# Kernel tuning notes

Measured on AMD Instinct MI355X. Metric: run time of the kernel, lower is better.

The kernel has to match this reference:

```python
import jax, jax.numpy as jnp
import numpy as np

EPS = 1e-5

def _bn(h, gamma, beta):
    # BatchNorm1d in training mode: per-channel stats over the batch dim (L=1)
    m = jnp.mean(h, axis=0)
    v = jnp.var(h, axis=0)  # biased variance, as torch uses for normalization
    return gamma * (h - m) * jax.lax.rsqrt(v + EPS) + beta

def setup_inputs() -> dict:
    key = jax.random.key(0)
    ks = jax.random.split(key, 8)
    vocab, emb = 8192, 512
    inter = (vocab + emb) // 2  # 4352
    N = 8192
    x_t = jax.random.randint(ks[0], (N,), 0, vocab, dtype=jnp.int64)
    W1 = jax.random.normal(ks[1], (inter, vocab), dtype=jnp.float32) * 0.02
    b1 = jax.random.normal(ks[2], (inter,), dtype=jnp.float32) * 0.02
    g1 = jnp.ones((inter,), dtype=jnp.float32)
    beta1 = jnp.zeros((inter,), dtype=jnp.float32)
    W2 = jax.random.normal(ks[3], (emb, inter), dtype=jnp.float32) * 0.02
    b2 = jax.random.normal(ks[4], (emb,), dtype=jnp.float32) * 0.02
    g2 = jnp.ones((emb,), dtype=jnp.float32)
    beta2 = jnp.zeros((emb,), dtype=jnp.float32)
    return {"x_t": x_t, "W1": W1, "b1": b1, "g1": g1, "beta1": beta1,
            "W2": W2, "b2": b2, "g2": g2, "beta2": beta2}

def reference(x_t, W1, b1, g1, beta1, W2, b2, g2, beta2):
    # one_hot(x_t) @ Conv1d(k=1) weight == gather of W1 columns (same math, no dense one-hot)
    h1 = W1.T[x_t] + b1                      # [N, inter]
    h1 = jax.nn.gelu(_bn(h1, g1, beta1), approximate=False)
    h2 = h1 @ W2.T + b2                      # [N, emb]
    out = jax.nn.gelu(_bn(h2, g2, beta2), approximate=False)
    return out
```

## Files before the change

### kernel.cpp

```cpp
#include <hip/hip_runtime.h>
#include <hip/hip_bf16.h>
#include <math.h>

typedef __attribute__((ext_vector_type(8))) short short8;
typedef __attribute__((ext_vector_type(4))) float f32x4;

#define VOCAB 8192
#define NSAMP 8192
#define INTER 4352
#define EMB   512

#define OFF_CNT    0
#define OFF_A1     32768
#define OFF_M1     50176
#define OFF_A2     67584
#define OFF_M2     69632
#define OFF_PS1B   71680
#define OFF_DONE   333824
#define OFF_PS2B   1120256
#define OFF_W2B    2168832
#define OFF_HACT   6625280
#define OFF_H2     77928448

__device__ __forceinline__ float gelu_exact(float x) {
    return 0.5f * x * (1.0f + erff(x * 0.70710678118654752f));
}
__device__ __forceinline__ unsigned short f2bf(float x) {
    __hip_bfloat16 b = __float2bfloat16(x);
    return *reinterpret_cast<unsigned short*>(&b);
}
__device__ __forceinline__ void async16(const unsigned short* g, unsigned short* l) {
    __builtin_amdgcn_global_load_lds(
        (const __attribute__((address_space(1))) void*)g,
        (__attribute__((address_space(3))) void*)l, 16, 0, 0);
}

__global__ __launch_bounds__(1024) void k_hist1b(const int* __restrict__ xt,
                                                 int* __restrict__ cnt,
                                                 unsigned* __restrict__ done) {
    __shared__ int h[VOCAB];
    const int t = threadIdx.x;
    #pragma unroll
    for (int i = 0; i < 8; ++i) h[t + i * 1024] = 0;
    if (t == 0) *done = 0u;
    __syncthreads();
    const int4* x4 = (const int4*)xt;
    int4 a = x4[t], b = x4[t + 1024];
    atomicAdd(&h[a.x], 1); atomicAdd(&h[a.y], 1);
    atomicAdd(&h[a.z], 1); atomicAdd(&h[a.w], 1);
    atomicAdd(&h[b.x], 1); atomicAdd(&h[b.y], 1);
    atomicAdd(&h[b.z], 1); atomicAdd(&h[b.w], 1);
    __syncthreads();
    #pragma unroll
    for (int i = 0; i < 2; ++i)
        ((int4*)cnt)[t + i * 1024] = ((const int4*)h)[t + i * 1024];
}

__global__ __launch_bounds__(256) void k_stats1(const float* __restrict__ W1,
                                                const int* __restrict__ cnt,
                                                const float* __restrict__ g1,
                                                float* __restrict__ a1,
                                                float* __restrict__ m1) {
    const int t = threadIdx.x, lane = t & 63, w = t >> 6;
    const int row = blockIdx.x * 4 + w;
    const float* wr = W1 + (size_t)row * VOCAB;
    float s1 = 0.f, s2 = 0.f;
    #pragma unroll 8
    for (int it = 0; it < 32; ++it) {
        int v = it * 256 + lane * 4;
        float4 x = *(const float4*)(wr + v);
        int4 c = *(const int4*)(cnt + v);
        float cx = (float)c.x, cy = (float)c.y, cz = (float)c.z, cw = (float)c.w;
        s1 += cx * x.x + cy * x.y + cz * x.z + cw * x.w;
        s2 += cx * x.x * x.x + cy * x.y * x.y + cz * x.z * x.z + cw * x.w * x.w;
    }
    #pragma unroll
    for (int d = 1; d < 64; d <<= 1) {
        s1 += __shfl_xor(s1, d);
        s2 += __shfl_xor(s2, d);
    }
    if (lane == 0) {
        float m = s1 * (1.f / NSAMP);
        float var = s2 * (1.f / NSAMP) - m * m;
        a1[row] = g1[row] * rsqrtf(var + 1e-5f);
        m1[row] = m;
    }
}

__global__ __launch_bounds__(256) void k_buildw2(const float* __restrict__ W1,
                                                 const float* __restrict__ a1,
                                                 const float* __restrict__ m1,
                                                 const float* __restrict__ beta1,
                                                 unsigned short* __restrict__ Hact,
                                                 const float* __restrict__ W2,
                                                 unsigned short* __restrict__ W2b) {
    const int bx = blockIdx.x;
    const int t = threadIdx.x;
    if (bx >= 2176) {
        int idx = ((bx - 2176) * 256 + t) * 4;
        float4 w = *(const float4*)(W2 + idx);
        ushort4 u;
        u.x = f2bf(w.x); u.y = f2bf(w.y); u.z = f2bf(w.z); u.w = f2bf(w.w);
        *(ushort4*)(W2b + idx) = u;
        return;
    }
    const int i0 = (bx % 68) * 64;
    const int v0 = (bx / 68) * 256;
    const int c0 = (t & 15) * 4;
    const int vg = (t >> 4) * 4;
    float4 av = *(const float4*)(a1 + i0 + c0);
    float4 mv = *(const float4*)(m1 + i0 + c0);
    float4 bv = *(const float4*)(beta1 + i0 + c0);
    const float* ap = (const float*)&av;
    const float* mp = (const float*)&mv;
    const float* bp = (const float*)&bv;
    #pragma unroll
    for (int vi = 0; vi < 4; ++vi) {
        int vb = v0 + vi * 64 + vg;
        float wf[4][4];
        #pragma unroll
        for (int j = 0; j < 4; ++j)
            *(float4*)&wf[j][0] = *(const float4*)(W1 + (size_t)(i0 + c0 + j) * VOCAB + vb);
        #pragma unroll
        for (int k = 0; k < 4; ++k) {
            ushort4 o;
            o.x = f2bf(gelu_exact(ap[0] * (wf[0][k] - mp[0]) + bp[0]));
            o.y = f2bf(gelu_exact(ap[1] * (wf[1][k] - mp[1]) + bp[1]));
            o.z = f2bf(gelu_exact(ap[2] * (wf[2][k] - mp[2]) + bp[2]));
            o.w = f2bf(gelu_exact(ap[3] * (wf[3][k] - mp[3]) + bp[3]));
            *(ushort4*)&Hact[(size_t)(vb + k) * INTER + i0 + c0] = o;
        }
    }
}

__global__ __launch_bounds__(256) void k_gemm(const unsigned short* __restrict__ A,
                                              const unsigned short* __restrict__ B,
                                              const int* __restrict__ cnt,
                                              float* __restrict__ h2,
                                              float* __restrict__ ps1,
                                              float* __restrict__ ps2,
                                              const float* __restrict__ g2,
                                              float* __restrict__ a2,
                                              float* __restrict__ m2,
                                              unsigned* __restrict__ done) {
    __shared__ __align__(16) unsigned short sA[2][128 * 64];
    __shared__ __align__(16) unsigned short sB[2][64 * 64];
    const int bid = blockIdx.x;
    const int mblk = bid & 63;
    const int nblk = bid >> 6;
    const int m0 = mblk * 128;
    const int n0 = nblk * 64;
    const int t = threadIdx.x;
    const int lane = t & 63;
    const int wave = t >> 6;
    const int wr = wave >> 1, wc = wave & 1;
    const int mq = lane & 15, kq = lane >> 4;
    const int srow = lane >> 3;
    const int sgrp = lane & 7;
    const int scol = (sgrp ^ srow) * 8;
    const int swz = mq & 7;

    const unsigned short* Ab = A + (size_t)(m0 + wave * 32 + srow) * INTER + scol;
    const unsigned short* Bb = B + (size_t)(n0 + wave * 16 + srow) * INTER + scol;

    f32x4 acc[4][2];
    #pragma unroll
    for (int r = 0; r < 4; ++r)
        #pragma unroll
        for (int c = 0; c < 2; ++c) acc[r][c] = (f32x4){0.f, 0.f, 0.f, 0.f};

    auto stage = [&](int buf, int tile) {
        const int k0 = tile * 64;
        #pragma unroll
        for (int p = 0; p < 4; ++p)
            async16(Ab + (size_t)(p * 8) * INTER + k0, &sA[buf][(wave * 32 + p * 8) * 64]);
        #pragma unroll
        for (int p = 0; p < 2; ++p)
            async16(Bb + (size_t)(p * 8) * INTER + k0, &sB[buf][(wave * 16 + p * 8) * 64]);
    };
    auto compute = [&](int buf) {
        #pragma unroll
        for (int kk = 0; kk < 64; kk += 32) {
            const int gbase = kq + (kk >> 3);
            short8 af[4], bfr[2];
            #pragma unroll
            for (int r = 0; r < 4; ++r)
                af[r] = *(const short8*)&sA[buf][(wr * 64 + r * 16 + mq) * 64 + ((gbase ^ swz) * 8)];
            #pragma unroll
            for (int c = 0; c < 2; ++c)
                bfr[c] = *(const short8*)&sB[buf][(wc * 32 + c * 16 + mq) * 64 + ((gbase ^ swz) * 8)];
            __builtin_amdgcn_s_setprio(1);
            #pragma unroll
            for (int r = 0; r < 4; ++r)
                #pragma unroll
                for (int c = 0; c < 2; ++c)
                    acc[r][c] = __builtin_amdgcn_mfma_f32_16x16x32_bf16(af[r], bfr[c], acc[r][c], 0, 0, 0);
            __builtin_amdgcn_s_setprio(0);
        }
    };

    stage(0, 0);
    __syncthreads();
    #pragma unroll 1
    for (int ti = 0; ti < 67; ++ti) {
        stage((ti + 1) & 1, ti + 1);
        compute(ti & 1);
        __syncthreads();
    }
    compute(1);

    float s1[2] = {0.f, 0.f}, s2[2] = {0.f, 0.f};
    #pragma unroll
    for (int r = 0; r < 4; ++r) {
        const int rowb = m0 + wr * 64 + r * 16 + kq * 4;
        int4 cw = *(const int4*)(cnt + rowb);
        float w0 = (float)cw.x, w1 = (float)cw.y, w2 = (float)cw.z, w3 = (float)cw.w;
        #pragma unroll
        for (int c = 0; c < 2; ++c) {
            const int col = n0 + wc * 32 + c * 16 + mq;
            float v0 = acc[r][c][0], v1 = acc[r][c][1], v2 = acc[r][c][2], v3 = acc[r][c][3];
            h2[(size_t)(rowb + 0) * EMB + col] = v0;
            h2[(size_t)(rowb + 1) * EMB + col] = v1;
            h2[(size_t)(rowb + 2) * EMB + col] = v2;
            h2[(size_t)(rowb + 3) * EMB + col] = v3;
            s1[c] += w0 * v0 + w1 * v1 + w2 * v2 + w3 * v3;
            s2[c] += w0 * v0 * v0 + w1 * v1 * v1 + w2 * v2 * v2 + w3 * v3 * v3;
        }
    }
    #pragma unroll
    for (int c = 0; c < 2; ++c) {
        s1[c] += __shfl_xor(s1[c], 16);
        s2[c] += __shfl_xor(s2[c], 16);
        s1[c] += __shfl_xor(s1[c], 32);
        s2[c] += __shfl_xor(s2[c], 32);
    }
    if (lane < 16) {
        const int slot = mblk * 2 + wr;
        #pragma unroll
        for (int c = 0; c < 2; ++c) {
            const int col = n0 + wc * 32 + c * 16 + mq;
            ps1[(size_t)col * 128 + slot] = s1[c];
            ps2[(size_t)col * 128 + slot] = s2[c];
        }
    }

    __shared__ bool sLast;
    __syncthreads();
    if (t == 0) {
        __threadfence();
        sLast = (atomicAdd(done, 1u) == 511u);
    }
    __syncthreads();
    if (sLast) {
        __threadfence();
        #pragma unroll
        for (int e = t; e < 512; e += 256) {
            float f1 = 0.f, f2 = 0.f;
            const float4* p1 = (const float4*)(ps1 + (size_t)e * 128);
            const float4* p2 = (const float4*)(ps2 + (size_t)e * 128);
            #pragma unroll 8
            for (int i = 0; i < 32; ++i) {
                float4 u = p1[i]; f1 += u.x + u.y + u.z + u.w;
                float4 v = p2[i]; f2 += v.x + v.y + v.z + v.w;
            }
            float m = f1 * (1.f / NSAMP);
            float var = f2 * (1.f / NSAMP) - m * m;
            a2[e] = g2[e] * rsqrtf(var + 1e-5f);
            m2[e] = m;
        }
    }
}

__global__ __launch_bounds__(256) void k_final(const float* __restrict__ h2,
                                               const int* __restrict__ xt,
                                               const float* __restrict__ a2,
                                               const float* __restrict__ m2,
                                               const float* __restrict__ beta2,
                                               float* __restrict__ out) {
    const int t = threadIdx.x;
    const int n = blockIdx.x * 2 + (t >> 7);
    const int e = (t & 127) * 4;
    const int v = xt[n];
    float4 h = *(const float4*)(h2 + (size_t)v * EMB + e);
    float4 a = *(const float4*)(a2 + e);
    float4 m = *(const float4*)(m2 + e);
    float4 b = *(const float4*)(beta2 + e);
    float4 o;
    o.x = gelu_exact(a.x * (h.x - m.x) + b.x);
    o.y = gelu_exact(a.y * (h.y - m.y) + b.y);
    o.z = gelu_exact(a.z * (h.z - m.z) + b.z);
    o.w = gelu_exact(a.w * (h.w - m.w) + b.w);
    *(float4*)(out + (size_t)n * EMB + e) = o;
}

extern "C" void kernel_launch(void* const* d_in, const int* in_sizes, int n_in,
                              void* d_out, int out_size, void* d_ws, size_t ws_size,
                              hipStream_t stream) {
    const int* xt      = (const int*)d_in[0];
    const float* W1    = (const float*)d_in[1];
    const float* g1    = (const float*)d_in[3];
    const float* beta1 = (const float*)d_in[4];
    const float* W2    = (const float*)d_in[5];
    const float* g2    = (const float*)d_in[7];
    const float* beta2 = (const float*)d_in[8];
    float* out = (float*)d_out;

    char* ws = (char*)d_ws;
    int*   cnt  = (int*)  (ws + OFF_CNT);
    float* a1   = (float*)(ws + OFF_A1);
    float* m1   = (float*)(ws + OFF_M1);
    float* a2   = (float*)(ws + OFF_A2);
    float* m2   = (float*)(ws + OFF_M2);
    float* ps1b = (float*)(ws + OFF_PS1B);
    float* ps2b = (float*)(ws + OFF_PS2B);
    unsigned* done = (unsigned*)(ws + OFF_DONE);
    unsigned short* W2b  = (unsigned short*)(ws + OFF_W2B);
    unsigned short* Hact = (unsigned short*)(ws + OFF_HACT);
    float* h2   = (float*)(ws + OFF_H2);

    k_hist1b<<<1, 1024, 0, stream>>>(xt, cnt, done);
    k_stats1<<<1088, 256, 0, stream>>>(W1, cnt, g1, a1, m1);
    k_buildw2<<<4352, 256, 0, stream>>>(W1, a1, m1, beta1, Hact, W2, W2b);
    k_gemm<<<512, 256, 0, stream>>>(Hact, W2b, cnt, h2, ps1b, ps2b, g2, a2, m2, done);
    k_final<<<4096, 256, 0, stream>>>(h2, xt, a2, m2, beta2, out);
}
```

Baseline: 368.4 us.

## Split GEMM over K with two partials and last-arriver reduction; larger N tile

The bf16 GEMM now uses a 128x128 tile with 512 threads and can split the K dimension in two. Each split writes its own partial output, and the second block to arrive for a tile sums both partials and runs the epilogue (stats and the h2 write). The single-block histogram kernel is replaced by a global-atomic histogram plus memsets, and h2 rows with zero count are no longer written. The aim is more blocks in flight and less per-block serial K work, at the cost of writing and reading an extra partial buffer, more atomics and two extra launches.

```diff
diff --git a/kernel.cpp b/kernel.cpp
--- a/kernel.cpp
+++ b/kernel.cpp
@@ -16,11 +16,12 @@
 #define OFF_A2     67584
 #define OFF_M2     69632
 #define OFF_PS1B   71680
-#define OFF_DONE   333824
+#define OFF_FLAGS  333824
 #define OFF_PS2B   1120256
 #define OFF_W2B    2168832
 #define OFF_HACT   6625280
 #define OFF_H2     77928448
+#define PART_BYTES 16777216ULL
 
 __device__ __forceinline__ float gelu_exact(float x) {
     return 0.5f * x * (1.0f + erff(x * 0.70710678118654752f));
@@ -35,25 +36,9 @@
         (__attribute__((address_space(3))) void*)l, 16, 0, 0);
 }
 
-__global__ __launch_bounds__(1024) void k_hist1b(const int* __restrict__ xt,
-                                                 int* __restrict__ cnt,
-                                                 unsigned* __restrict__ done) {
-    __shared__ int h[VOCAB];
-    const int t = threadIdx.x;
-    #pragma unroll
-    for (int i = 0; i < 8; ++i) h[t + i * 1024] = 0;
-    if (t == 0) *done = 0u;
-    __syncthreads();
-    const int4* x4 = (const int4*)xt;
-    int4 a = x4[t], b = x4[t + 1024];
-    atomicAdd(&h[a.x], 1); atomicAdd(&h[a.y], 1);
-    atomicAdd(&h[a.z], 1); atomicAdd(&h[a.w], 1);
-    atomicAdd(&h[b.x], 1); atomicAdd(&h[b.y], 1);
-    atomicAdd(&h[b.z], 1); atomicAdd(&h[b.w], 1);
-    __syncthreads();
-    #pragma unroll
-    for (int i = 0; i < 2; ++i)
-        ((int4*)cnt)[t + i * 1024] = ((const int4*)h)[t + i * 1024];
+__global__ void k_hist(const int* __restrict__ xt, int* __restrict__ cnt) {
+    int n = blockIdx.x * 256 + threadIdx.x;
+    atomicAdd(&cnt[xt[n]], 1);
 }
 
 __global__ __launch_bounds__(256) void k_stats1(const float* __restrict__ W1,
@@ -133,35 +118,41 @@
     }
 }
 
-__global__ __launch_bounds__(256) void k_gemm(const unsigned short* __restrict__ A,
+__global__ __launch_bounds__(512) void k_gemm(const unsigned short* __restrict__ A,
                                               const unsigned short* __restrict__ B,
                                               const int* __restrict__ cnt,
+                                              float* __restrict__ hpart,
                                               float* __restrict__ h2,
                                               float* __restrict__ ps1,
                                               float* __restrict__ ps2,
                                               const float* __restrict__ g2,
                                               float* __restrict__ a2,
                                               float* __restrict__ m2,
-                                              unsigned* __restrict__ done) {
+                                              unsigned* __restrict__ flags,
+                                              int kPer, int S) {
     __shared__ __align__(16) unsigned short sA[2][128 * 64];
-    __shared__ __align__(16) unsigned short sB[2][64 * 64];
+    __shared__ __align__(16) unsigned short sB[2][128 * 64];
     const int bid = blockIdx.x;
     const int mblk = bid & 63;
-    const int nblk = bid >> 6;
+    const int nblk = (bid >> 6) & 3;
+    const int ks   = bid >> 8;
     const int m0 = mblk * 128;
-    const int n0 = nblk * 64;
+    const int n0 = nblk * 128;
+    const int kbeg = ks * kPer;
+    const int nsteps = kPer >> 6;
+    float* C = hpart + (size_t)ks * NSAMP * EMB;
     const int t = threadIdx.x;
     const int lane = t & 63;
     const int wave = t >> 6;
-    const int wr = wave >> 1, wc = wave & 1;
+    const int wr = wave >> 2, wc = wave & 3;
     const int mq = lane & 15, kq = lane >> 4;
     const int srow = lane >> 3;
     const int sgrp = lane & 7;
     const int scol = (sgrp ^ srow) * 8;
     const int swz = mq & 7;
 
-    const unsigned short* Ab = A + (size_t)(m0 + wave * 32 + srow) * INTER + scol;
-    const unsigned short* Bb = B + (size_t)(n0 + wave * 16 + srow) * INTER + scol;
+    const unsigned short* Ab = A + (size_t)(m0 + wave * 16 + srow) * INTER + kbeg + scol;
+    const unsigned short* Bb = B + (size_t)(n0 + wave * 16 + srow) * INTER + kbeg + scol;
 
     f32x4 acc[4][2];
     #pragma unroll
@@ -171,12 +162,10 @@
 
     auto stage = [&](int buf, int tile) {
         const int k0 = tile * 64;
-        #pragma unroll
-        for (int p = 0; p < 4; ++p)
-            async16(Ab + (size_t)(p * 8) * INTER + k0, &sA[buf][(wave * 32 + p * 8) * 64]);
-        #pragma unroll
-        for (int p = 0; p < 2; ++p)
-            async16(Bb + (size_t)(p * 8) * INTER + k0, &sB[buf][(wave * 16 + p * 8) * 64]);
+        async16(Ab + k0,                     &sA[buf][(wave * 16) * 64]);
+        async16(Ab + (size_t)8 * INTER + k0, &sA[buf][(wave * 16 + 8) * 64]);
+        async16(Bb + k0,                     &sB[buf][(wave * 16) * 64]);
+        async16(Bb + (size_t)8 * INTER + k0, &sB[buf][(wave * 16 + 8) * 64]);
     };
     auto compute = [&](int buf) {
         #pragma unroll
@@ -202,29 +191,60 @@
     stage(0, 0);
     __syncthreads();
     #pragma unroll 1
-    for (int ti = 0; ti < 67; ++ti) {
+    for (int ti = 0; ti < nsteps - 1; ++ti) {
         stage((ti + 1) & 1, ti + 1);
         compute(ti & 1);
         __syncthreads();
     }
-    compute(1);
-
+    compute((nsteps - 1) & 1);
+
+    #pragma unroll
+    for (int r = 0; r < 4; ++r) {
+        const int rowb = m0 + wr * 64 + r * 16 + kq * 4;
+        #pragma unroll
+        for (int c = 0; c < 2; ++c) {
+            const int col = n0 + wc * 32 + c * 16 + mq;
+            #pragma unroll
+            for (int j = 0; j < 4; ++j)
+                C[(size_t)(rowb + j) * EMB + col] = acc[r][c][j];
+        }
+    }
+
+    __shared__ bool sLoser, sLast;
+    if (S == 2) {
+        __syncthreads();
+        if (t == 0) {
+            __threadfence();
+            sLoser = (atomicAdd(&flags[bid & 255], 1u) == 1u);
+        }
+        __syncthreads();
+        if (!sLoser) return;
+        __threadfence();
+    }
+
+    const float* other = hpart + (size_t)(1 - ks) * NSAMP * EMB;
     float s1[2] = {0.f, 0.f}, s2[2] = {0.f, 0.f};
     #pragma unroll
     for (int r = 0; r < 4; ++r) {
         const int rowb = m0 + wr * 64 + r * 16 + kq * 4;
         int4 cw = *(const int4*)(cnt + rowb);
-        float w0 = (float)cw.x, w1 = (float)cw.y, w2 = (float)cw.z, w3 = (float)cw.w;
         #pragma unroll
         for (int c = 0; c < 2; ++c) {
             const int col = n0 + wc * 32 + c * 16 + mq;
             float v0 = acc[r][c][0], v1 = acc[r][c][1], v2 = acc[r][c][2], v3 = acc[r][c][3];
-            h2[(size_t)(rowb + 0) * EMB + col] = v0;
-            h2[(size_t)(rowb + 1) * EMB + col] = v1;
-            h2[(size_t)(rowb + 2) * EMB + col] = v2;
-            h2[(size_t)(rowb + 3) * EMB + col] = v3;
-            s1[c] += w0 * v0 + w1 * v1 + w2 * v2 + w3 * v3;
-            s2[c] += w0 * v0 * v0 + w1 * v1 * v1 + w2 * v2 * v2 + w3 * v3 * v3;
+            if (S == 2) {
+                v0 += other[(size_t)(rowb + 0) * EMB + col];
+                v1 += other[(size_t)(rowb + 1) * EMB + col];
+                v2 += other[(size_t)(rowb + 2) * EMB + col];
+                v3 += other[(size_t)(rowb + 3) * EMB + col];
+            }
+            if (cw.x > 0) h2[(size_t)(rowb + 0) * EMB + col] = v0;
+            if (cw.y > 0) h2[(size_t)(rowb + 1) * EMB + col] = v1;
+            if (cw.z > 0) h2[(size_t)(rowb + 2) * EMB + col] = v2;
+            if (cw.w > 0) h2[(size_t)(rowb + 3) * EMB + col] = v3;
+            float w0 = (float)cw.x, w1 = (float)cw.y, w2f = (float)cw.z, w3 = (float)cw.w;
+            s1[c] += w0 * v0 + w1 * v1 + w2f * v2 + w3 * v3;
+            s2[c] += w0 * v0 * v0 + w1 * v1 * v1 + w2f * v2 * v2 + w3 * v3 * v3;
         }
     }
     #pragma unroll
@@ -244,30 +264,26 @@
         }
     }
 
-    __shared__ bool sLast;
     __syncthreads();
     if (t == 0) {
         __threadfence();
-        sLast = (atomicAdd(done, 1u) == 511u);
+        sLast = (atomicAdd(&flags[256], 1u) == 255u);
     }
     __syncthreads();
     if (sLast) {
         __threadfence();
-        #pragma unroll
-        for (int e = t; e < 512; e += 256) {
-            float f1 = 0.f, f2 = 0.f;
-            const float4* p1 = (const float4*)(ps1 + (size_t)e * 128);
-            const float4* p2 = (const float4*)(ps2 + (size_t)e * 128);
-            #pragma unroll 8
-            for (int i = 0; i < 32; ++i) {
-                float4 u = p1[i]; f1 += u.x + u.y + u.z + u.w;
-                float4 v = p2[i]; f2 += v.x + v.y + v.z + v.w;
-            }
-            float m = f1 * (1.f / NSAMP);
-            float var = f2 * (1.f / NSAMP) - m * m;
-            a2[e] = g2[e] * rsqrtf(var + 1e-5f);
-            m2[e] = m;
-        }
+        float f1 = 0.f, f2 = 0.f;
+        const float4* p1 = (const float4*)(ps1 + (size_t)t * 128);
+        const float4* p2 = (const float4*)(ps2 + (size_t)t * 128);
+        #pragma unroll 8
+        for (int i = 0; i < 32; ++i) {
+            float4 u = p1[i]; f1 += u.x + u.y + u.z + u.w;
+            float4 v = p2[i]; f2 += v.x + v.y + v.z + v.w;
+        }
+        float m = f1 * (1.f / NSAMP);
+        float var = f2 * (1.f / NSAMP) - m * m;
+        a2[t] = g2[t] * rsqrtf(var + 1e-5f);
+        m2[t] = m;
     }
 }
 
@@ -313,14 +329,20 @@
     float* m2   = (float*)(ws + OFF_M2);
     float* ps1b = (float*)(ws + OFF_PS1B);
     float* ps2b = (float*)(ws + OFF_PS2B);
-    unsigned* done = (unsigned*)(ws + OFF_DONE);
+    unsigned* flags = (unsigned*)(ws + OFF_FLAGS);
     unsigned short* W2b  = (unsigned short*)(ws + OFF_W2B);
     unsigned short* Hact = (unsigned short*)(ws + OFF_HACT);
-    float* h2   = (float*)(ws + OFF_H2);
-
-    k_hist1b<<<1, 1024, 0, stream>>>(xt, cnt, done);
+    float* hpart = (float*)(ws + OFF_H2);
+    float* h2 = hpart;
+
+    const int S = (ws_size >= OFF_H2 + 2 * PART_BYTES) ? 2 : 1;
+
+    hipMemsetAsync(cnt, 0, VOCAB * sizeof(int), stream);
+    hipMemsetAsync(flags, 0, 257 * sizeof(unsigned), stream);
+    k_hist<<<32, 256, 0, stream>>>(xt, cnt);
     k_stats1<<<1088, 256, 0, stream>>>(W1, cnt, g1, a1, m1);
     k_buildw2<<<4352, 256, 0, stream>>>(W1, a1, m1, beta1, Hact, W2, W2b);
-    k_gemm<<<512, 256, 0, stream>>>(Hact, W2b, cnt, h2, ps1b, ps2b, g2, a2, m2, done);
+    k_gemm<<<256 * S, 512, 0, stream>>>(Hact, W2b, cnt, hpart, h2, ps1b, ps2b,
+                                        g2, a2, m2, flags, INTER / S, S);
     k_final<<<4096, 256, 0, stream>>>(h2, xt, a2, m2, beta2, out);
 }
```

New measurement: 397.4 us. 7.9% more time.
